# Performance work log

Measured on AMD Instinct MI355X. Metric: run time of the kernel, lower is better.

## Reference

```python
import jax, jax.numpy as jnp
import numpy as np

NB_RADIUSES = 24


def setup_inputs() -> dict:
    key = jax.random.key(0)
    # (nb, nf, nr, nz) radii per angle
    x = jax.random.uniform(key, (16, 8, NB_RADIUSES, 512), dtype=jnp.float32)
    return {"x": x}


def reference(x) -> jnp.ndarray:
    """Vectorized diameter extraction.

    For each (b, f, z) group, the nr radii define 2D points
    p_i = (r_i*cos(theta_i), r_i*sin(theta_i)); the diameter is the max
    pairwise Euclidean distance (== |complex_i - complex_j| in the original).
    """
    nb, nf, nr, nz = x.shape
    angles = jnp.arange(nr, dtype=x.dtype) * (2.0 * jnp.pi / nr) - jnp.pi  # (nr,)
    ca = jnp.cos(angles)[None, None, :, None]
    sa = jnp.sin(angles)[None, None, :, None]
    px = x * ca  # (nb, nf, nr, nz) real part
    py = x * sa  # (nb, nf, nr, nz) imag part
    # pairwise differences over the radius axis: (nb, nf, nr, nr, nz)
    dx = px[:, :, :, None, :] - px[:, :, None, :, :]
    dy = py[:, :, :, None, :] - py[:, :, None, :, :]
    dist = jnp.sqrt(dx * dx + dy * dy)
    return dist.max(axis=(2, 3))  # (nb, nf, nz)
```

## Files before the change

### kernel.cpp

```cpp
#include <hip/hip_runtime.h>

#define NR 24
#define NZ 512

__device__ __constant__ float C2[NR] = {
     2.0000000000000000f,  1.9318516525781366f,  1.7320508075688774f,
     1.4142135623730951f,  1.0000000000000000f,  0.5176380902050415f,
     0.0000000000000000f, -0.5176380902050415f, -1.0000000000000000f,
    -1.4142135623730951f, -1.7320508075688774f, -1.9318516525781366f,
    -2.0000000000000000f, -1.9318516525781366f, -1.7320508075688774f,
    -1.4142135623730951f, -1.0000000000000000f, -0.5176380902050415f,
     0.0000000000000000f,  0.5176380902050415f,  1.0000000000000000f,
     1.4142135623730951f,  1.7320508075688774f,  1.9318516525781366f
};

__global__ __launch_bounds__(256) void diam_kernel(const float* __restrict__ x,
                                                   float* __restrict__ out,
                                                   int total) {
    int o = blockIdx.x * blockDim.x + threadIdx.x;
    if (o >= total) return;

    int g = o >> 9;
    int z = o & (NZ - 1);
    const float* __restrict__ base = x + (size_t)g * NR * NZ + z;

    float rad[NR];
#pragma unroll
    for (int r = 0; r < NR; ++r) {
        rad[r] = base[r * NZ];
    }

    float r2[NR];
#pragma unroll
    for (int r = 0; r < NR; ++r) {
        r2[r] = rad[r] * rad[r];
    }

    float m = 0.0f;
#pragma unroll
    for (int i = 0; i < NR; ++i) {
#pragma unroll
        for (int j = i + 1; j < NR; ++j) {
            float d2 = fmaf(-C2[j - i], rad[i] * rad[j], r2[i] + r2[j]);
            m = fmaxf(m, d2);
        }
    }

    out[o] = sqrtf(m);
}

extern "C" void kernel_launch(void* const* d_in, const int* in_sizes, int n_in,
                              void* d_out, int out_size, void* d_ws, size_t ws_size,
                              hipStream_t stream) {
    const float* x = (const float*)d_in[0];
    float* out = (float*)d_out;
    int total = out_size;
    int block = 256;
    int grid = (total + block - 1) / block;
    diam_kernel<<<grid, block, 0, stream>>>(x, out, total);
}
```

Baseline: 9.722 us.

## Split pairwise max across two threads per output with shuffle reduction

Each output is now computed by two adjacent threads, which take alternating rows i of the pairwise loop and combine their maxima with a lane shuffle. The distance formula is reassociated into two FMAs per pair with the cosine table as a compile-time constexpr, and the inner loop is unrolled two-wide with a per-row partial max. This doubles thread count to raise occupancy and latency hiding, at the cost of both threads loading all 24 radii, doubling global reads, and splitting rows unevenly between the two halves. Both threads write the same output value.

```diff
diff --git a/kernel.cpp b/kernel.cpp
--- a/kernel.cpp
+++ b/kernel.cpp
@@ -3,7 +3,7 @@
 #define NR 24
 #define NZ 512
 
-__device__ __constant__ float C2[NR] = {
+constexpr float CC[NR] = {
      2.0000000000000000f,  1.9318516525781366f,  1.7320508075688774f,
      1.4142135623730951f,  1.0000000000000000f,  0.5176380902050415f,
      0.0000000000000000f, -0.5176380902050415f, -1.0000000000000000f,
@@ -16,10 +16,12 @@
 
 __global__ __launch_bounds__(256) void diam_kernel(const float* __restrict__ x,
                                                    float* __restrict__ out,
-                                                   int total) {
-    int o = blockIdx.x * blockDim.x + threadIdx.x;
-    if (o >= total) return;
+                                                   int total2) {
+    int t = blockIdx.x * blockDim.x + threadIdx.x;
+    if (t >= total2) return;
 
+    int o    = t >> 1;
+    int half = t & 1;
     int g = o >> 9;
     int z = o & (NZ - 1);
     const float* __restrict__ base = x + (size_t)g * NR * NZ + z;
@@ -30,22 +32,30 @@
         rad[r] = base[r * NZ];
     }
 
-    float r2[NR];
+    float m = 0.0f;
 #pragma unroll
-    for (int r = 0; r < NR; ++r) {
-        r2[r] = rad[r] * rad[r];
+    for (int i = 0; i < NR - 1; ++i) {
+        if ((i & 1) != half) continue;
+        float r2i = rad[i] * rad[i];
+        float mi = 0.0f;
+        int j = i + 1;
+#pragma unroll
+        for (; j + 1 < NR; j += 2) {
+            float ta  = fmaf(-CC[j - i],     rad[i], rad[j]);
+            float d2a = fmaf(rad[j],     ta, r2i);
+            float tb  = fmaf(-CC[j + 1 - i], rad[i], rad[j + 1]);
+            float d2b = fmaf(rad[j + 1], tb, r2i);
+            mi = fmaxf(mi, fmaxf(d2a, d2b));
+        }
+        if (j < NR) {
+            float tc  = fmaf(-CC[j - i], rad[i], rad[j]);
+            float d2c = fmaf(rad[j], tc, r2i);
+            mi = fmaxf(mi, d2c);
+        }
+        m = fmaxf(m, mi);
     }
 
-    float m = 0.0f;
-#pragma unroll
-    for (int i = 0; i < NR; ++i) {
-#pragma unroll
-        for (int j = i + 1; j < NR; ++j) {
-            float d2 = fmaf(-C2[j - i], rad[i] * rad[j], r2[i] + r2[j]);
-            m = fmaxf(m, d2);
-        }
-    }
-
+    m = fmaxf(m, __shfl_xor(m, 1));
     out[o] = sqrtf(m);
 }
 
@@ -54,8 +64,8 @@
                               hipStream_t stream) {
     const float* x = (const float*)d_in[0];
     float* out = (float*)d_out;
-    int total = out_size;
+    int total2 = out_size * 2;
     int block = 256;
-    int grid = (total + block - 1) / block;
-    diam_kernel<<<grid, block, 0, stream>>>(x, out, total);
+    int grid = (total2 + block - 1) / block;
+    diam_kernel<<<grid, block, 0, stream>>>(x, out, total2);
 }
```

Measured after the change: 9.711 us. Within noise of the previous version (-0.1%).
